# Kernel tuning notes

Measured on AMD Instinct MI355X. Metric: run time of the kernel, lower is better.

The kernel has to match this reference:

```python
import jax, jax.numpy as jnp
import numpy as np
import math

H, NH, DH, FF = 768, 12, 64, 3072
B, S = 8, 1024

def _gelu(x):
    return x * 0.5 * (1.0 + jax.lax.erf(x / math.sqrt(2.0)))

def _layernorm(x, gamma, beta, eps=1e-6):
    mean = jnp.mean(x, axis=-1, keepdims=True)
    std = jnp.std(x, axis=-1, keepdims=True, ddof=1)  # torch unbiased std
    return gamma * (x - mean) / (std + eps) + beta

def setup_inputs() -> dict:
    key = jax.random.key(0)
    ks = jax.random.split(key, 16)
    p = lambda k, shape: jax.random.normal(k, shape, dtype=jnp.float32) * 0.02
    return {
        "hidden": jax.random.normal(ks[0], (B, S, H), dtype=jnp.float32),
        "mask": jnp.zeros((B, 1, S, S), dtype=jnp.float32),
        "position_bias": jax.random.normal(ks[1], (1, NH, S, S), dtype=jnp.float32),
        "Wq": p(ks[2], (H, H)), "bq": jnp.zeros((H,), jnp.float32),
        "Wk": p(ks[3], (H, H)), "bk": jnp.zeros((H,), jnp.float32),
        "Wv": p(ks[4], (H, H)), "bv": jnp.zeros((H,), jnp.float32),
        "Wo": p(ks[5], (H, H)), "bo": jnp.zeros((H,), jnp.float32),
        "W1": p(ks[6], (H, FF)), "b1": jnp.zeros((FF,), jnp.float32),
        "W2": p(ks[7], (FF, H)), "b2": jnp.zeros((H,), jnp.float32),
        "g1": jnp.ones((H,), jnp.float32), "beta1": jnp.zeros((H,), jnp.float32),
        "g2": jnp.ones((H,), jnp.float32), "beta2": jnp.zeros((H,), jnp.float32),
    }

def reference(hidden, mask, position_bias, Wq, bq, Wk, bk, Wv, bv, Wo, bo,
              W1, b1, W2, b2, g1, beta1, g2, beta2):
    b, s, _ = hidden.shape
    def split_heads(x):
        return x.reshape(b, s, NH, DH).transpose(0, 2, 1, 3)  # [b, h, s, d]
    q = split_heads(hidden @ Wq + bq)
    k = split_heads(hidden @ Wk + bk)
    v = split_heads(hidden @ Wv + bv)
    scores = jnp.einsum('bhqd,bhkd->bhqk', q, k)
    scores = scores + position_bias          # bias added BEFORE scaling (as in source)
    scores = scores / math.sqrt(float(DH))
    scores = scores + mask
    probs = jax.nn.softmax(scores, axis=-1)  # dropout is identity in eval
    ctx = jnp.einsum('bhqk,bhkd->bhqd', probs, v)
    ctx = ctx.transpose(0, 2, 1, 3).reshape(b, s, NH * DH)
    attn_out = ctx @ Wo + bo
    inter = _layernorm(attn_out + hidden, g1, beta1)
    ffn = _gelu(inter @ W1 + b1) @ W2 + b2
    return _layernorm(ffn + inter, g2, beta2)
```

## Files before the change

### kernel.cpp

```cpp
#include <hip/hip_runtime.h>
#include <cmath>

typedef __bf16 bf16;
typedef __attribute__((ext_vector_type(8))) __bf16 bf16x8;
typedef __attribute__((ext_vector_type(4))) __bf16 bf16x4;
typedef __attribute__((ext_vector_type(4))) float f32x4;

#define DEVINL __device__ __forceinline__

DEVINL void gload16(const void* g, void* l) {
    __builtin_amdgcn_global_load_lds((const __attribute__((address_space(1))) void*)g,
                                     (__attribute__((address_space(3))) void*)l, 16, 0, 0);
}


__global__ void cast_bf16_kernel(const float* __restrict__ in, bf16* __restrict__ out, int n4) {
    int i = blockIdx.x * 256 + threadIdx.x;
    if (i < n4) {
        float4 v = ((const float4*)in)[i];
        bf16x4 o;
        o[0] = (bf16)v.x; o[1] = (bf16)v.y; o[2] = (bf16)v.z; o[3] = (bf16)v.w;
        ((bf16x4*)out)[i] = o;
    }
}

__global__ void prep_pm_kernel(const float* __restrict__ pb, const float* __restrict__ mask,
                               bf16* __restrict__ pbs, bf16* __restrict__ maskb,
                               int n1, int n2) {
    const int i = blockIdx.x * 256 + threadIdx.x;
    const float c1 = 0.18033688011112042f;
    const float c2 = 1.4426950408889634f;
    if (i < n1) {
        float4 v = ((const float4*)pb)[i];
        bf16x4 o;
        o[0] = (bf16)(v.x * c1); o[1] = (bf16)(v.y * c1);
        o[2] = (bf16)(v.z * c1); o[3] = (bf16)(v.w * c1);
        ((bf16x4*)pbs)[i] = o;
    } else if (i < n1 + n2) {
        const int j = i - n1;
        float4 v = ((const float4*)mask)[j];
        bf16x4 o;
        o[0] = (bf16)(v.x * c2); o[1] = (bf16)(v.y * c2);
        o[2] = (bf16)(v.z * c2); o[3] = (bf16)(v.w * c2);
        ((bf16x4*)maskb)[j] = o;
    }
}

__global__ void tcast_kernel(const float* __restrict__ in, bf16* __restrict__ out, int R, int C) {
    __shared__ float t[32][33];
    int tx = threadIdx.x & 31, ty = threadIdx.x >> 5;
    int r0 = blockIdx.y * 32, c0 = blockIdx.x * 32;
#pragma unroll
    for (int i = 0; i < 4; ++i)
        t[ty + 8 * i][tx] = in[(size_t)(r0 + ty + 8 * i) * C + c0 + tx];
    __syncthreads();
#pragma unroll
    for (int i = 0; i < 4; ++i)
        out[(size_t)(c0 + ty + 8 * i) * R + r0 + tx] = (bf16)t[tx][ty + 8 * i];
}

__global__ void concat_bias_kernel(const float* __restrict__ a, const float* __restrict__ b,
                                   const float* __restrict__ c, float* __restrict__ out) {
    int i = blockIdx.x * 256 + threadIdx.x;
    if (i < 2304) out[i] = (i < 768) ? a[i] : ((i < 1536) ? b[i - 768] : c[i - 1536]);
}

__global__ __launch_bounds__(256) void vtrans_kernel(const bf16* __restrict__ qkv,
                                                     bf16* __restrict__ vT) {
    __shared__ bf16 t[64][72];
    const int tid = threadIdx.x;
    const int bh = blockIdx.y, s0 = blockIdx.x * 32;
    const int b = bh / 12, h = bh % 12;
    {
        const int r = tid >> 3, c8 = (tid & 7) * 8;
        bf16x8 v = *(const bf16x8*)(qkv + (size_t)(b * 1024 + s0 + r) * 2304 + 1536 + h * 64 + c8);
#pragma unroll
        for (int j = 0; j < 8; ++j) t[c8 + j][r] = v[j];
    }
    __syncthreads();
    {
        const int d = tid >> 2, s8 = (tid & 3) * 8;
        bf16x8 o = *(const bf16x8*)(&t[d][s8]);
        *(bf16x8*)(vT + (size_t)(bh * 64 + d) * 1024 + s0 + s8) = o;
    }
}

template<int MODE>
__global__ __launch_bounds__(256, 4) void gemm_kernel(const bf16* __restrict__ A, const bf16* __restrict__ Bt,
                                                      const float* __restrict__ bias,
                                                      bf16* __restrict__ Cb, float* __restrict__ Cf,
                                                      int M, int N, int K, int ldc) {
    __shared__ __align__(16) bf16 As[128 * 64];
    __shared__ __align__(16) bf16 Bs[128 * 64];
    const int tid = threadIdx.x;
    const int wid = tid >> 6, lane = tid & 63;
    const int L = blockIdx.y * gridDim.x + blockIdx.x;
    const int cpx = (gridDim.x * gridDim.y) >> 3;
    const int wg = (L & 7) * cpx + (L >> 3);
    const int m0 = (wg / gridDim.x) * 128, n0 = (wg % gridDim.x) * 128;
    const int wr = (wid >> 1) * 64, wc = (wid & 1) * 64;
    const int lg = lane >> 4, l15 = lane & 15;
    f32x4 acc[4][4] = {};

    for (int k0 = 0; k0 < K; k0 += 64) {
        __syncthreads();
#pragma unroll
        for (int i = 0; i < 4; ++i) {
            const int cbase = (wid * 4 + i) * 1024;
            const int td = cbase + lane * 16;
            const int row = td >> 7;
            const int s16 = ((td >> 4) & 7) ^ (row & 7);
            gload16(A + (size_t)(m0 + row) * K + k0 + s16 * 8, (char*)As + cbase);
            gload16(Bt + (size_t)(n0 + row) * K + k0 + s16 * 8, (char*)Bs + cbase);
        }
        __syncthreads();
#pragma unroll
        for (int kk = 0; kk < 2; ++kk) {
            bf16x8 af[4], bfr[4];
#pragma unroll
            for (int mi = 0; mi < 4; ++mi) {
                int ra = wr + mi * 16 + l15;
                int off = (ra * 128 + (kk * 32 + 8 * lg) * 2) ^ ((ra & 7) << 4);
                af[mi] = *(const bf16x8*)((const char*)As + off);
            }
#pragma unroll
            for (int ni = 0; ni < 4; ++ni) {
                int rb = wc + ni * 16 + l15;
                int off = (rb * 128 + (kk * 32 + 8 * lg) * 2) ^ ((rb & 7) << 4);
                bfr[ni] = *(const bf16x8*)((const char*)Bs + off);
            }
#pragma unroll
            for (int mi = 0; mi < 4; ++mi)
#pragma unroll
                for (int ni = 0; ni < 4; ++ni)
                    acc[mi][ni] = __builtin_amdgcn_mfma_f32_16x16x32_bf16(af[mi], bfr[ni], acc[mi][ni], 0, 0, 0);
        }
    }
#pragma unroll
    for (int mi = 0; mi < 4; ++mi) {
#pragma unroll
        for (int r = 0; r < 4; ++r) {
            const int row = m0 + wr + mi * 16 + lg * 4 + r;
#pragma unroll
            for (int ni = 0; ni < 4; ++ni) {
                const int col = n0 + wc + ni * 16 + l15;
                float v = acc[mi][ni][r] + bias[col];
                if (MODE == 2) v = v * 0.5f * (1.0f + erff(v * 0.70710678118654752f));
                if (MODE == 1) Cf[(size_t)row * ldc + col] = v;
                else           Cb[(size_t)row * ldc + col] = (bf16)v;
            }
        }
    }
}

__global__ __launch_bounds__(256, 3) void attn_kernel(const bf16* __restrict__ qkv,
                                                      const bf16* __restrict__ pbs,
                                                      const bf16* __restrict__ maskb,
                                                      const bf16* __restrict__ vT,
                                                      bf16* __restrict__ ctx) {
    __shared__ __align__(16) bf16 Kb[3][64 * 64];
    __shared__ __align__(16) bf16 Vb[3][64 * 64];
    const int tid = threadIdx.x, wid = tid >> 6, lane = tid & 63;
    const int bh = blockIdx.y, b = bh / 12, h = bh % 12;
    const int q0 = blockIdx.x * 128 + wid * 32;
    const int lg = lane >> 4, l15 = lane & 15;
    const float cqk = 0.18033688011112042f;

    bf16x8 aq[2][2];
#pragma unroll
    for (int qs = 0; qs < 2; ++qs) {
        const size_t r = (size_t)(b * 1024 + q0 + qs * 16 + l15) * 2304 + h * 64 + 8 * lg;
        aq[qs][0] = *(const bf16x8*)(qkv + r);
        aq[qs][1] = *(const bf16x8*)(qkv + r + 32);
    }

    auto stage = [&](int tt, int pp) {
#pragma unroll
        for (int rd = 0; rd < 2; ++rd) {
            const int n = rd * 256 + tid;
            const int i = n >> 3, sl = n & 7, c = sl ^ (i & 7);
            const int sig = (i & 32) | ((i & 12) << 1) | ((i & 16) >> 2) | (i & 3);
            gload16(qkv + (size_t)(b * 1024 + tt * 64 + sig) * 2304 + 768 + h * 64 + c * 8,
                    (char*)Kb[pp] + (rd * 256 + wid * 64) * 16);
            gload16(vT + ((size_t)bh * 64 + i) * 1024 + tt * 64 + c * 8,
                    (char*)Vb[pp] + (rd * 256 + wid * 64) * 16);
        }
    };

    float mrun[2] = {-1e30f, -1e30f}, lsum[2] = {0.f, 0.f};
    f32x4 acc[2][4] = {};

    stage(0, 0);
    stage(1, 1);
    __syncthreads();
    for (int t = 0; t < 16; ++t) {
        const int p = t % 3;
        const int k0 = t * 64;
        bf16x8 pbv[2][2], mkv[2][2];
#pragma unroll
        for (int qs = 0; qs < 2; ++qs) {
            const int q = q0 + qs * 16 + l15;
            const bf16* pr = pbs + ((size_t)h * 1024 + q) * 1024 + k0 + lg * 8;
            const bf16* mr = maskb + ((size_t)b * 1024 + q) * 1024 + k0 + lg * 8;
            pbv[qs][0] = *(const bf16x8*)pr;  pbv[qs][1] = *(const bf16x8*)(pr + 32);
            mkv[qs][0] = *(const bf16x8*)mr;  mkv[qs][1] = *(const bf16x8*)(mr + 32);
        }
        if (t < 14) stage(t + 2, (t + 2) % 3);

        bf16x8 bk[4][2];
#pragma unroll
        for (int kt = 0; kt < 4; ++kt) {
            const int row = kt * 16 + l15;
            const int byte = (row * 128 + lg * 16) ^ ((row & 7) << 4);
            bk[kt][0] = *(const bf16x8*)((const char*)Kb[p] + byte);
            bk[kt][1] = *(const bf16x8*)((const char*)Kb[p] + (byte ^ 64));
        }
        f32x4 s[2][4];
#pragma unroll
        for (int qs = 0; qs < 2; ++qs)
#pragma unroll
            for (int kt = 0; kt < 4; ++kt) {
                f32x4 z = {};
                z = __builtin_amdgcn_mfma_f32_16x16x32_bf16(bk[kt][0], aq[qs][0], z, 0, 0, 0);
                z = __builtin_amdgcn_mfma_f32_16x16x32_bf16(bk[kt][1], aq[qs][1], z, 0, 0, 0);
                s[qs][kt] = z;
            }
#pragma unroll
        for (int qs = 0; qs < 2; ++qs)
#pragma unroll
            for (int kt = 0; kt < 4; ++kt)
#pragma unroll
                for (int r = 0; r < 4; ++r) {
                    const int j = (kt & 1) * 4 + r;
                    s[qs][kt][r] = s[qs][kt][r] * cqk
                                 + (float)pbv[qs][kt >> 1][j]
                                 + (float)mkv[qs][kt >> 1][j];
                }
        bf16x8 po[2][2];
#pragma unroll
        for (int qs = 0; qs < 2; ++qs) {
            float tm = s[qs][0][0];
#pragma unroll
            for (int kt = 0; kt < 4; ++kt)
#pragma unroll
                for (int r = 0; r < 4; ++r) tm = fmaxf(tm, s[qs][kt][r]);
            tm = fmaxf(tm, __shfl_xor(tm, 16));
            tm = fmaxf(tm, __shfl_xor(tm, 32));
            if (!__all(tm <= mrun[qs] + 6.0f)) {
                const float mn = fmaxf(mrun[qs], tm);
                const float scal = __builtin_amdgcn_exp2f(mrun[qs] - mn);
                mrun[qs] = mn;
                lsum[qs] *= scal;
#pragma unroll
                for (int dt = 0; dt < 4; ++dt) {
                    acc[qs][dt][0] *= scal; acc[qs][dt][1] *= scal;
                    acc[qs][dt][2] *= scal; acc[qs][dt][3] *= scal;
                }
            }
            float ts = 0.f;
#pragma unroll
            for (int kt = 0; kt < 4; ++kt)
#pragma unroll
                for (int r = 0; r < 4; ++r) {
                    const float pv = __builtin_amdgcn_exp2f(s[qs][kt][r] - mrun[qs]);
                    ts += pv;
                    const int idx = kt * 4 + r;
                    if (idx < 8) po[qs][0][idx] = (bf16)pv;
                    else         po[qs][1][idx - 8] = (bf16)pv;
                }
            ts += __shfl_xor(ts, 16);
            ts += __shfl_xor(ts, 32);
            lsum[qs] += ts;
        }
        bf16x8 vb[4][2];
#pragma unroll
        for (int dt = 0; dt < 4; ++dt) {
            const int row = dt * 16 + l15;
            const int byte = (row * 128 + lg * 16) ^ ((row & 7) << 4);
            vb[dt][0] = *(const bf16x8*)((const char*)Vb[p] + byte);
            vb[dt][1] = *(const bf16x8*)((const char*)Vb[p] + (byte ^ 64));
        }
#pragma unroll
        for (int qs = 0; qs < 2; ++qs)
#pragma unroll
            for (int dt = 0; dt < 4; ++dt) {
                acc[qs][dt] = __builtin_amdgcn_mfma_f32_16x16x32_bf16(vb[dt][0], po[qs][0], acc[qs][dt], 0, 0, 0);
                acc[qs][dt] = __builtin_amdgcn_mfma_f32_16x16x32_bf16(vb[dt][1], po[qs][1], acc[qs][dt], 0, 0, 0);
            }
        __syncthreads();
    }
    char* scr = (char*)Kb + wid * 4096;
#pragma unroll
    for (int qs = 0; qs < 2; ++qs) {
        const float inv = 1.0f / lsum[qs];
        const int ql = qs * 16 + l15;
#pragma unroll
        for (int dt = 0; dt < 4; ++dt) {
            bf16x4 o;
#pragma unroll
            for (int r = 0; r < 4; ++r) o[r] = (bf16)(acc[qs][dt][r] * inv);
            const int wb = (ql * 128 + dt * 32 + lg * 8) ^ ((ql & 7) << 4);
            *(bf16x4*)(scr + wb) = o;
        }
    }
    __syncthreads();
#pragma unroll
    for (int qs = 0; qs < 2; ++qs) {
        const int ql = qs * 16 + l15;
        const int rb = (ql * 128 + lg * 32) ^ ((ql & 7) << 4);
        bf16x8 o0 = *(const bf16x8*)(scr + rb);
        bf16x8 o1 = *(const bf16x8*)(scr + (rb ^ 16));
        bf16* cp = ctx + (size_t)(b * 1024 + q0 + ql) * 768 + h * 64 + lg * 16;
        *(bf16x8*)cp = o0;
        *(bf16x8*)(cp + 8) = o1;
    }
}

template<int MODE>
__global__ __launch_bounds__(256) void ln_kernel(const float* __restrict__ x,
                                                 const float* __restrict__ resf,
                                                 const bf16* __restrict__ resb,
                                                 const float* __restrict__ g, const float* __restrict__ bt,
                                                 float* __restrict__ outf, bf16* __restrict__ outb) {
    const int wid = threadIdx.x >> 6, lane = threadIdx.x & 63;
    const int row = blockIdx.x * 4 + wid;
    const float4* xr = (const float4*)(x + (size_t)row * 768);
    float4 v[3];
    float s = 0.f, ss = 0.f;
#pragma unroll
    for (int j = 0; j < 3; ++j) {
        float4 a = xr[lane + 64 * j];
        float4 b;
        if (MODE == 0) {
            b = ((const float4*)(resf + (size_t)row * 768))[lane + 64 * j];
        } else {
            bf16x4 rb = ((const bf16x4*)(resb + (size_t)row * 768))[lane + 64 * j];
            b.x = (float)rb[0]; b.y = (float)rb[1]; b.z = (float)rb[2]; b.w = (float)rb[3];
        }
        float4 w;
        w.x = a.x + b.x; w.y = a.y + b.y; w.z = a.z + b.z; w.w = a.w + b.w;
        v[j] = w;
        s += w.x + w.y + w.z + w.w;
        ss += w.x * w.x + w.y * w.y + w.z * w.z + w.w * w.w;
    }
#pragma unroll
    for (int off = 1; off <= 32; off <<= 1) { s += __shfl_xor(s, off); ss += __shfl_xor(ss, off); }
    const float mean = s * (1.f / 768.f);
    float var = (ss - 768.f * mean * mean) * (1.f / 767.f);
    var = fmaxf(var, 0.f);
    const float inv = 1.f / (sqrtf(var) + 1e-6f);
#pragma unroll
    for (int j = 0; j < 3; ++j) {
        float4 gv = ((const float4*)g)[lane + 64 * j];
        float4 bv = ((const float4*)bt)[lane + 64 * j];
        float4 y;
        y.x = gv.x * (v[j].x - mean) * inv + bv.x;
        y.y = gv.y * (v[j].y - mean) * inv + bv.y;
        y.z = gv.z * (v[j].z - mean) * inv + bv.z;
        y.w = gv.w * (v[j].w - mean) * inv + bv.w;
        if (MODE == 1) {
            ((float4*)(outf + (size_t)row * 768))[lane + 64 * j] = y;
        } else {
            bf16x4 o;
            o[0] = (bf16)y.x; o[1] = (bf16)y.y; o[2] = (bf16)y.z; o[3] = (bf16)y.w;
            ((bf16x4*)(outb + (size_t)row * 768))[lane + 64 * j] = o;
        }
    }
}


extern "C" void kernel_launch(void* const* d_in, const int* in_sizes, int n_in,
                              void* d_out, int out_size, void* d_ws, size_t ws_size,
                              hipStream_t stream) {
    const float* hidden = (const float*)d_in[0];
    const float* mask   = (const float*)d_in[1];
    const float* pb     = (const float*)d_in[2];
    const float* Wq = (const float*)d_in[3];
    const float* bq = (const float*)d_in[4];
    const float* Wk = (const float*)d_in[5];
    const float* bk = (const float*)d_in[6];
    const float* Wv = (const float*)d_in[7];
    const float* bv = (const float*)d_in[8];
    const float* Wo = (const float*)d_in[9];
    const float* bo = (const float*)d_in[10];
    const float* W1 = (const float*)d_in[11];
    const float* b1 = (const float*)d_in[12];
    const float* W2 = (const float*)d_in[13];
    const float* b2 = (const float*)d_in[14];
    const float* g1  = (const float*)d_in[15];
    const float* be1 = (const float*)d_in[16];
    const float* g2  = (const float*)d_in[17];
    const float* be2 = (const float*)d_in[18];
    float* out = (float*)d_out;

    char* ws = (char*)d_ws;
    bf16*  xbf     = (bf16*)(ws);
    bf16*  wqkv_t  = (bf16*)(ws + 12582912);
    bf16*  wo_t    = (bf16*)(ws + 16121856);
    bf16*  w1_t    = (bf16*)(ws + 17301504);
    bf16*  w2_t    = (bf16*)(ws + 22020096);
    float* bqkv    = (float*)(ws + 26738688);
    bf16*  qkv     = (bf16*)(ws + 26747904);
    bf16*  ffn1    = qkv;
    bf16*  vT      = (bf16*)(ws + 26747904 + 37748736);
    bf16*  ctx     = (bf16*)(ws + 77079552);
    float* attn_out= (float*)(ws + 89662464);
    bf16*  pbs     = (bf16*)(ws + 89662464);
    float* ffn2    = attn_out;
    bf16*  maskb   = (bf16*)(ws + 114828288);
    bf16*  interb  = xbf;

    cast_bf16_kernel<<<6291456 / 4 / 256, 256, 0, stream>>>(hidden, xbf, 6291456 / 4);
    tcast_kernel<<<dim3(24, 24), 256, 0, stream>>>(Wq, wqkv_t, 768, 768);
    tcast_kernel<<<dim3(24, 24), 256, 0, stream>>>(Wk, wqkv_t + 768 * 768, 768, 768);
    tcast_kernel<<<dim3(24, 24), 256, 0, stream>>>(Wv, wqkv_t + 2 * 768 * 768, 768, 768);
    tcast_kernel<<<dim3(24, 24), 256, 0, stream>>>(Wo, wo_t, 768, 768);
    tcast_kernel<<<dim3(96, 24), 256, 0, stream>>>(W1, w1_t, 768, 3072);
    tcast_kernel<<<dim3(24, 96), 256, 0, stream>>>(W2, w2_t, 3072, 768);
    concat_bias_kernel<<<9, 256, 0, stream>>>(bq, bk, bv, bqkv);
    prep_pm_kernel<<<(3145728 + 2097152) / 256, 256, 0, stream>>>(pb, mask, pbs, maskb,
                                                                  3145728, 2097152);

    gemm_kernel<0><<<dim3(18, 64), 256, 0, stream>>>(xbf, wqkv_t, bqkv, qkv, nullptr, 8192, 2304, 768, 2304);
    vtrans_kernel<<<dim3(32, 96), 256, 0, stream>>>(qkv, vT);
    attn_kernel<<<dim3(8, 96), 256, 0, stream>>>(qkv, pbs, maskb, vT, ctx);
    gemm_kernel<1><<<dim3(6, 64), 256, 0, stream>>>(ctx, wo_t, bo, nullptr, attn_out, 8192, 768, 768, 768);
    ln_kernel<0><<<2048, 256, 0, stream>>>(attn_out, hidden, nullptr, g1, be1, nullptr, interb);
    gemm_kernel<2><<<dim3(24, 64), 256, 0, stream>>>(interb, w1_t, b1, ffn1, nullptr, 8192, 3072, 768, 3072);
    gemm_kernel<1><<<dim3(6, 64), 256, 0, stream>>>(ffn1, w2_t, b2, nullptr, ffn2, 8192, 768, 3072, 768);
    ln_kernel<1><<<2048, 256, 0, stream>>>(ffn2, nullptr, interb, g2, be2, out, nullptr);
}
```

Baseline: 330.0 us.

## Narrow N-tile for 768-wide GEMMs, swap attention grid, prefetch bias/mask

Templates the GEMM on tile width BN and uses 64-wide tiles for the two N=768 GEMMs. This doubles their block count (384 to 768) so more of the GPU's CUs have work. The attention grid is transposed so consecutive blocks cover different heads and batches instead of query tiles of the same head. The attention loop is unrolled by two with double-buffered register prefetch of the position-bias and mask tiles one iteration ahead, to hide their global-load latency. The narrower tiles cut data reuse per block and the extra registers may lower occupancy.

```diff
diff --git a/kernel.cpp b/kernel.cpp
--- a/kernel.cpp
+++ b/kernel.cpp
@@ -85,22 +85,24 @@
     }
 }
 
-template<int MODE>
+template<int MODE, int BN>
 __global__ __launch_bounds__(256, 4) void gemm_kernel(const bf16* __restrict__ A, const bf16* __restrict__ Bt,
                                                       const float* __restrict__ bias,
                                                       bf16* __restrict__ Cb, float* __restrict__ Cf,
                                                       int M, int N, int K, int ldc) {
+    constexpr int NI = BN / 32;
+    constexpr int BLOADS = BN / 32;
     __shared__ __align__(16) bf16 As[128 * 64];
-    __shared__ __align__(16) bf16 Bs[128 * 64];
+    __shared__ __align__(16) bf16 Bs[BN * 64];
     const int tid = threadIdx.x;
     const int wid = tid >> 6, lane = tid & 63;
     const int L = blockIdx.y * gridDim.x + blockIdx.x;
     const int cpx = (gridDim.x * gridDim.y) >> 3;
     const int wg = (L & 7) * cpx + (L >> 3);
-    const int m0 = (wg / gridDim.x) * 128, n0 = (wg % gridDim.x) * 128;
-    const int wr = (wid >> 1) * 64, wc = (wid & 1) * 64;
+    const int m0 = (wg / gridDim.x) * 128, n0 = (wg % gridDim.x) * BN;
+    const int wr = (wid >> 1) * 64, wc = (wid & 1) * (BN / 2);
     const int lg = lane >> 4, l15 = lane & 15;
-    f32x4 acc[4][4] = {};
+    f32x4 acc[4][NI] = {};
 
     for (int k0 = 0; k0 < K; k0 += 64) {
         __syncthreads();
@@ -111,12 +113,19 @@
             const int row = td >> 7;
             const int s16 = ((td >> 4) & 7) ^ (row & 7);
             gload16(A + (size_t)(m0 + row) * K + k0 + s16 * 8, (char*)As + cbase);
+        }
+#pragma unroll
+        for (int i = 0; i < BLOADS; ++i) {
+            const int cbase = (wid * BLOADS + i) * 1024;
+            const int td = cbase + lane * 16;
+            const int row = td >> 7;
+            const int s16 = ((td >> 4) & 7) ^ (row & 7);
             gload16(Bt + (size_t)(n0 + row) * K + k0 + s16 * 8, (char*)Bs + cbase);
         }
         __syncthreads();
 #pragma unroll
         for (int kk = 0; kk < 2; ++kk) {
-            bf16x8 af[4], bfr[4];
+            bf16x8 af[4], bfr[NI];
 #pragma unroll
             for (int mi = 0; mi < 4; ++mi) {
                 int ra = wr + mi * 16 + l15;
@@ -124,7 +133,7 @@
                 af[mi] = *(const bf16x8*)((const char*)As + off);
             }
 #pragma unroll
-            for (int ni = 0; ni < 4; ++ni) {
+            for (int ni = 0; ni < NI; ++ni) {
                 int rb = wc + ni * 16 + l15;
                 int off = (rb * 128 + (kk * 32 + 8 * lg) * 2) ^ ((rb & 7) << 4);
                 bfr[ni] = *(const bf16x8*)((const char*)Bs + off);
@@ -132,7 +141,7 @@
 #pragma unroll
             for (int mi = 0; mi < 4; ++mi)
 #pragma unroll
-                for (int ni = 0; ni < 4; ++ni)
+                for (int ni = 0; ni < NI; ++ni)
                     acc[mi][ni] = __builtin_amdgcn_mfma_f32_16x16x32_bf16(af[mi], bfr[ni], acc[mi][ni], 0, 0, 0);
         }
     }
@@ -142,7 +151,7 @@
         for (int r = 0; r < 4; ++r) {
             const int row = m0 + wr + mi * 16 + lg * 4 + r;
 #pragma unroll
-            for (int ni = 0; ni < 4; ++ni) {
+            for (int ni = 0; ni < NI; ++ni) {
                 const int col = n0 + wc + ni * 16 + l15;
                 float v = acc[mi][ni][r] + bias[col];
                 if (MODE == 2) v = v * 0.5f * (1.0f + erff(v * 0.70710678118654752f));
@@ -161,8 +170,8 @@
     __shared__ __align__(16) bf16 Kb[3][64 * 64];
     __shared__ __align__(16) bf16 Vb[3][64 * 64];
     const int tid = threadIdx.x, wid = tid >> 6, lane = tid & 63;
-    const int bh = blockIdx.y, b = bh / 12, h = bh % 12;
-    const int q0 = blockIdx.x * 128 + wid * 32;
+    const int bh = blockIdx.x, b = bh / 12, h = bh % 12;
+    const int q0 = blockIdx.y * 128 + wid * 32;
     const int lg = lane >> 4, l15 = lane & 15;
     const float cqk = 0.18033688011112042f;
 
@@ -187,16 +196,8 @@
         }
     };
 
-    float mrun[2] = {-1e30f, -1e30f}, lsum[2] = {0.f, 0.f};
-    f32x4 acc[2][4] = {};
-
-    stage(0, 0);
-    stage(1, 1);
-    __syncthreads();
-    for (int t = 0; t < 16; ++t) {
-        const int p = t % 3;
+    auto loadpm = [&](int t, bf16x8 (&pbv)[2][2], bf16x8 (&mkv)[2][2]) {
         const int k0 = t * 64;
-        bf16x8 pbv[2][2], mkv[2][2];
 #pragma unroll
         for (int qs = 0; qs < 2; ++qs) {
             const int q = q0 + qs * 16 + l15;
@@ -205,8 +206,12 @@
             pbv[qs][0] = *(const bf16x8*)pr;  pbv[qs][1] = *(const bf16x8*)(pr + 32);
             mkv[qs][0] = *(const bf16x8*)mr;  mkv[qs][1] = *(const bf16x8*)(mr + 32);
         }
-        if (t < 14) stage(t + 2, (t + 2) % 3);
-
+    };
+
+    float mrun[2] = {-1e30f, -1e30f}, lsum[2] = {0.f, 0.f};
+    f32x4 acc[2][4] = {};
+
+    auto tile = [&](int p, bf16x8 (&pbv)[2][2], bf16x8 (&mkv)[2][2]) {
         bf16x8 bk[4][2];
 #pragma unroll
         for (int kt = 0; kt < 4; ++kt) {
@@ -287,6 +292,21 @@
                 acc[qs][dt] = __builtin_amdgcn_mfma_f32_16x16x32_bf16(vb[dt][0], po[qs][0], acc[qs][dt], 0, 0, 0);
                 acc[qs][dt] = __builtin_amdgcn_mfma_f32_16x16x32_bf16(vb[dt][1], po[qs][1], acc[qs][dt], 0, 0, 0);
             }
+    };
+
+    bf16x8 pA[2][2], mA[2][2], pB[2][2], mB[2][2];
+    stage(0, 0);
+    stage(1, 1);
+    loadpm(0, pA, mA);
+    __syncthreads();
+    for (int tt = 0; tt < 16; tt += 2) {
+        loadpm(tt + 1, pB, mB);
+        if (tt + 2 < 16) stage(tt + 2, (tt + 2) % 3);
+        tile(tt % 3, pA, mA);
+        __syncthreads();
+        if (tt + 2 < 16) loadpm(tt + 2, pA, mA);
+        if (tt + 3 < 16) stage(tt + 3, (tt + 3) % 3);
+        tile((tt + 1) % 3, pB, mB);
         __syncthreads();
     }
     char* scr = (char*)Kb + wid * 4096;
@@ -421,12 +441,12 @@
     prep_pm_kernel<<<(3145728 + 2097152) / 256, 256, 0, stream>>>(pb, mask, pbs, maskb,
                                                                   3145728, 2097152);
 
-    gemm_kernel<0><<<dim3(18, 64), 256, 0, stream>>>(xbf, wqkv_t, bqkv, qkv, nullptr, 8192, 2304, 768, 2304);
+    gemm_kernel<0, 128><<<dim3(18, 64), 256, 0, stream>>>(xbf, wqkv_t, bqkv, qkv, nullptr, 8192, 2304, 768, 2304);
     vtrans_kernel<<<dim3(32, 96), 256, 0, stream>>>(qkv, vT);
-    attn_kernel<<<dim3(8, 96), 256, 0, stream>>>(qkv, pbs, maskb, vT, ctx);
-    gemm_kernel<1><<<dim3(6, 64), 256, 0, stream>>>(ctx, wo_t, bo, nullptr, attn_out, 8192, 768, 768, 768);
+    attn_kernel<<<dim3(96, 8), 256, 0, stream>>>(qkv, pbs, maskb, vT, ctx);
+    gemm_kernel<1, 64><<<dim3(12, 64), 256, 0, stream>>>(ctx, wo_t, bo, nullptr, attn_out, 8192, 768, 768, 768);
     ln_kernel<0><<<2048, 256, 0, stream>>>(attn_out, hidden, nullptr, g1, be1, nullptr, interb);
-    gemm_kernel<2><<<dim3(24, 64), 256, 0, stream>>>(interb, w1_t, b1, ffn1, nullptr, 8192, 3072, 768, 3072);
-    gemm_kernel<1><<<dim3(6, 64), 256, 0, stream>>>(ffn1, w2_t, b2, nullptr, ffn2, 8192, 768, 3072, 768);
+    gemm_kernel<2, 128><<<dim3(24, 64), 256, 0, stream>>>(interb, w1_t, b1, ffn1, nullptr, 8192, 3072, 768, 3072);
+    gemm_kernel<1, 64><<<dim3(12, 64), 256, 0, stream>>>(ffn1, w2_t, b2, nullptr, ffn2, 8192, 768, 3072, 768);
     ln_kernel<1><<<2048, 256, 0, stream>>>(ffn2, nullptr, interb, g2, be2, out, nullptr);
 }
```

Measured after the change: 384.3 us. +16.5%, slower.
